# Kernel optimization log

Hardware: AMD Instinct MI355X
Metric: run time of the kernel (lower is better)

## Reference

```python
import jax, jax.numpy as jnp
import numpy as np

N_NODES = 200000
N_EDGES = 4000000

# SE3 layout (pypose convention): [tx, ty, tz, qx, qy, qz, qw]

def _qmul(q, r):
    x1, y1, z1, w1 = q[..., 0], q[..., 1], q[..., 2], q[..., 3]
    x2, y2, z2, w2 = r[..., 0], r[..., 1], r[..., 2], r[..., 3]
    return jnp.stack([
        w1 * x2 + x1 * w2 + y1 * z2 - z1 * y2,
        w1 * y2 - x1 * z2 + y1 * w2 + z1 * x2,
        w1 * z2 + x1 * y2 - y1 * x2 + z1 * w2,
        w1 * w2 - x1 * x2 - y1 * y2 - z1 * z2,
    ], axis=-1)


def _qrot(q, v):
    # rotate vector v by unit quaternion q: v + w*t + qv x t, t = 2 qv x v
    qv, w = q[..., :3], q[..., 3:4]
    t = 2.0 * jnp.cross(qv, v)
    return v + w * t + jnp.cross(qv, t)


def _se3_inv(T):
    t, q = T[..., :3], T[..., 3:]
    qi = q * jnp.asarray([-1.0, -1.0, -1.0, 1.0], dtype=T.dtype)
    ti = -_qrot(qi, t)
    return jnp.concatenate([ti, qi], axis=-1)


def _se3_mul(T1, T2):
    t1, q1 = T1[..., :3], T1[..., 3:]
    t2, q2 = T2[..., :3], T2[..., 3:]
    return jnp.concatenate([t1 + _qrot(q1, t2), _qmul(q1, q2)], axis=-1)


def _se3_log(T):
    # SE3 Log -> se3 [rho(3), phi(3)] (pypose order: translational part first)
    t, q = T[..., :3], T[..., 3:]
    # canonicalize quaternion to w >= 0 (shortest rotation)
    q = jnp.where(q[..., 3:4] < 0, -q, q)
    qv, w = q[..., :3], q[..., 3]
    n = jnp.linalg.norm(qv, axis=-1)           # sin(theta/2)
    theta = 2.0 * jnp.arctan2(n, w)            # rotation angle in [0, pi]
    small = n < 1e-6
    safe_n = jnp.where(small, 1.0, n)
    # phi = theta * axis ; small-angle: 2/w (Taylor of 2*atan2(n,w)/n)
    scale = jnp.where(small, 2.0 / jnp.maximum(w, 1e-12), theta / safe_n)
    phi = scale[..., None] * qv
    # rho = Jl(phi)^{-1} t
    th2 = theta * theta
    tiny = theta < 1e-4
    safe_th = jnp.where(tiny, 1.0, theta)
    coef = jnp.where(
        tiny,
        1.0 / 12.0 + th2 / 720.0,
        1.0 / jnp.where(tiny, 1.0, th2)
        - (1.0 + jnp.cos(safe_th)) / (2.0 * safe_th * jnp.sin(safe_th)),
    )
    pxt = jnp.cross(phi, t)
    rho = t - 0.5 * pxt + coef[..., None] * jnp.cross(phi, pxt)
    return jnp.concatenate([rho, phi], axis=-1)


def _random_se3(key, n):
    kt, kq = jax.random.split(key)
    t = jax.random.normal(kt, (n, 3), dtype=jnp.float32)
    q = jax.random.normal(kq, (n, 4), dtype=jnp.float32)
    q = q / jnp.linalg.norm(q, axis=-1, keepdims=True)
    return jnp.concatenate([t, q], axis=-1)


def setup_inputs() -> dict:
    key = jax.random.key(0)
    k1, k2, k3 = jax.random.split(key, 3)
    nodes = _random_se3(k1, N_NODES)            # [N, 7]
    poses = _random_se3(k2, N_EDGES)            # [E, 7]
    edges = jax.random.randint(k3, (N_EDGES, 2), 0, N_NODES, dtype=jnp.int64)
    return {"nodes": nodes, "poses": poses, "edges": edges}


def reference(nodes, poses, edges):
    node1 = nodes[edges[..., 0]]                # [E, 7] gather
    node2 = nodes[edges[..., 1]]                # [E, 7] gather
    error = _se3_mul(_se3_mul(poses, _se3_inv(node1)), node2)
    return _se3_log(error)                      # [E, 6]
```

## Files before the change

kernel.cpp:

```cpp
#include <hip/hip_runtime.h>

constexpr int BLK = 256;
constexpr int EPT = 2;
constexpr int EPB = BLK * EPT;

struct F3 { float x, y, z; };
struct F4 { float x, y, z, w; };

__device__ __forceinline__ F3 cross3(const F3 a, const F3 b) {
    return { a.y * b.z - a.z * b.y,
             a.z * b.x - a.x * b.z,
             a.x * b.y - a.y * b.x };
}

__device__ __forceinline__ F3 qrot(const F4 q, const F3 v) {
    F3 qv{ q.x, q.y, q.z };
    F3 t = cross3(qv, v);
    t.x *= 2.f; t.y *= 2.f; t.z *= 2.f;
    F3 c = cross3(qv, t);
    return { v.x + q.w * t.x + c.x,
             v.y + q.w * t.y + c.y,
             v.z + q.w * t.z + c.z };
}

__device__ __forceinline__ F4 qmul(const F4 a, const F4 b) {
    return { a.w * b.x + a.x * b.w + a.y * b.z - a.z * b.y,
             a.w * b.y - a.x * b.z + a.y * b.w + a.z * b.x,
             a.w * b.z + a.x * b.y - a.y * b.x + a.z * b.w,
             a.w * b.w - a.x * b.x - a.y * b.y - a.z * b.z };
}

__device__ __forceinline__ void edge_compute(const F3 tp, const F4 qp,
                                             const float4 nA0, const float4 nA1,
                                             const float4 nB0, const float4 nB1,
                                             float* __restrict__ o)
{
    F3 t1{ nA0.x, nA0.y, nA0.z };
    F4 q1{ nA0.w, nA1.x, nA1.y, nA1.z };
    F3 t2{ nB0.x, nB0.y, nB0.z };
    F4 q2{ nB0.w, nB1.x, nB1.y, nB1.z };

    F4 qi{ -q1.x, -q1.y, -q1.z, q1.w };
    F3 ti = qrot(qi, t1);
    ti.x = -ti.x; ti.y = -ti.y; ti.z = -ti.z;

    F3 ra = qrot(qp, ti);
    F3 tA{ tp.x + ra.x, tp.y + ra.y, tp.z + ra.z };
    F4 qA = qmul(qp, qi);

    F3 rb = qrot(qA, t2);
    F3 tE{ tA.x + rb.x, tA.y + rb.y, tA.z + rb.z };
    F4 qE = qmul(qA, q2);

    if (qE.w < 0.f) { qE.x = -qE.x; qE.y = -qE.y; qE.z = -qE.z; qE.w = -qE.w; }
    const float n2q = qE.x * qE.x + qE.y * qE.y + qE.z * qE.z;
    const float nq = sqrtf(n2q);
    const float theta = 2.f * atan2f(nq, qE.w);
    const bool small = nq < 1e-6f;
    const float scale = small ? (2.f / fmaxf(qE.w, 1e-12f)) : (theta / nq);
    const F3 phi{ scale * qE.x, scale * qE.y, scale * qE.z };

    const float th2 = theta * theta;
    float coef;
    if (theta < 1e-4f) {
        coef = 1.f / 12.f + th2 / 720.f;
    } else {
        coef = 1.f / th2 - (1.f + cosf(theta)) / (2.f * theta * sinf(theta));
    }

    const F3 pxt  = cross3(phi, tE);
    const F3 ppxt = cross3(phi, pxt);
    o[0] = tE.x - 0.5f * pxt.x + coef * ppxt.x;
    o[1] = tE.y - 0.5f * pxt.y + coef * ppxt.y;
    o[2] = tE.z - 0.5f * pxt.z + coef * ppxt.z;
    o[3] = phi.x; o[4] = phi.y; o[5] = phi.z;
}

__global__ __launch_bounds__(BLK) void pad_nodes_kernel(
    const float* __restrict__ nodes, float* __restrict__ ws, int n_nodes)
{
    int i = blockIdx.x * BLK + threadIdx.x;
    if (i < n_nodes) {
        const float* s = nodes + (size_t)i * 7;
        float4 a{ s[0], s[1], s[2], s[3] };
        float4 b{ s[4], s[5], s[6], 0.f };
        float4* d = (float4*)(ws + (size_t)i * 8);
        d[0] = a; d[1] = b;
    }
}

template<int NS>
__device__ __forceinline__ void load_node(const float* __restrict__ nodes, int idx,
                                          float4& a, float4& b)
{
    if (NS == 8) {
        const float4* g = (const float4*)(nodes + (size_t)idx * 8);
        a = g[0]; b = g[1];
    } else {
        const float* g = nodes + (size_t)idx * 7;
        a = { g[0], g[1], g[2], g[3] };
        b = { g[4], g[5], g[6], 0.f };
    }
}

template<int NS>
__global__ __launch_bounds__(BLK) void pose_graph_err_kernel(
    const float* __restrict__ nodes,
    const float* __restrict__ poses,
    const int*   __restrict__ edges,
    float*       __restrict__ out,
    int n_edges)
{
    __shared__ float s_pose[EPB * 7];

    const int tid = threadIdx.x;
    const long long bstart = (long long)blockIdx.x * EPB;
    const long long remain = (long long)n_edges - bstart;

    if (remain >= EPB) {
        const float4* pv = (const float4*)(poses + bstart * 7);
        float4* sp = (float4*)s_pose;
        #pragma unroll
        for (int i = tid; i < EPB * 7 / 4; i += BLK) sp[i] = pv[i];

        const long long e0 = bstart + (long long)tid * EPT;
        const int4 ij = *(const int4*)(edges + e0 * 2);

        float4 nA0, nA1, nB0, nB1, nC0, nC1, nD0, nD1;
        load_node<NS>(nodes, ij.x, nA0, nA1);
        load_node<NS>(nodes, ij.y, nB0, nB1);
        load_node<NS>(nodes, ij.z, nC0, nC1);
        load_node<NS>(nodes, ij.w, nD0, nD1);

        __syncthreads();

        const float* p0 = s_pose + tid * 14;
        F3 tp0{ p0[0], p0[1], p0[2] };
        F4 qp0{ p0[3], p0[4], p0[5], p0[6] };
        F3 tp1{ p0[7], p0[8], p0[9] };
        F4 qp1{ p0[10], p0[11], p0[12], p0[13] };

        union { float4 v[3]; float f[12]; } O;
        edge_compute(tp0, qp0, nA0, nA1, nB0, nB1, &O.f[0]);
        edge_compute(tp1, qp1, nC0, nC1, nD0, nD1, &O.f[6]);

        float4* ov = (float4*)(out + e0 * 6);
        ov[0] = O.v[0]; ov[1] = O.v[1]; ov[2] = O.v[2];
    } else {
        for (int k = 0; k < EPT; ++k) {
            const long long e = bstart + tid + (long long)k * BLK;
            if (e < n_edges) {
                const float* sp = poses + e * 7;
                F3 tp{ sp[0], sp[1], sp[2] };
                F4 qp{ sp[3], sp[4], sp[5], sp[6] };
                float4 a0, a1, b0, b1;
                load_node<NS>(nodes, edges[e*2],   a0, a1);
                load_node<NS>(nodes, edges[e*2+1], b0, b1);
                float o[6];
                edge_compute(tp, qp, a0, a1, b0, b1, o);
                #pragma unroll
                for (int j = 0; j < 6; ++j) out[e*6+j] = o[j];
            }
        }
    }
}

extern "C" void kernel_launch(void* const* d_in, const int* in_sizes, int n_in,
                              void* d_out, int out_size, void* d_ws, size_t ws_size,
                              hipStream_t stream) {
    const float* nodes = (const float*)d_in[0];
    const float* poses = (const float*)d_in[1];
    const int*   edges = (const int*)d_in[2];
    float* out = (float*)d_out;

    const int n_nodes = in_sizes[0] / 7;
    const int n_edges = in_sizes[2] / 2;
    const int nblocks = (n_edges + EPB - 1) / EPB;

    const size_t pad_bytes = (size_t)n_nodes * 8 * sizeof(float);
    if (ws_size >= pad_bytes) {
        float* nodes8 = (float*)d_ws;
        pad_nodes_kernel<<<(n_nodes + BLK - 1) / BLK, BLK, 0, stream>>>(nodes, nodes8, n_nodes);
        pose_graph_err_kernel<8><<<nblocks, BLK, 0, stream>>>(nodes8, poses, edges, out, n_edges);
    } else {
        pose_graph_err_kernel<7><<<nblocks, BLK, 0, stream>>>(nodes, poses, edges, out, n_edges);
    }
}
```

Measured before the change: 124.5 us.

## Use one edge per thread, stage outputs in LDS, drop sin/cos in log

Each thread now handles one edge instead of two. Outputs are staged in shared memory and written back with coalesced float4 stores. The rotation coefficient uses the identity (1+cos θ)/sin θ = w/n, taken from the quaternion, so the cosf/sinf calls are no longer needed. This trades the extra per-thread edge parallelism for more blocks and an additional barrier plus an LDS round trip, and it removes costly transcendental calls from the compute path.

```diff
diff --git a/kernel.cpp b/kernel.cpp
--- a/kernel.cpp
+++ b/kernel.cpp
@@ -1,8 +1,6 @@
 #include <hip/hip_runtime.h>
 
 constexpr int BLK = 256;
-constexpr int EPT = 2;
-constexpr int EPB = BLK * EPT;
 
 struct F3 { float x, y, z; };
 struct F4 { float x, y, z, w; };
@@ -56,17 +54,14 @@
     const float n2q = qE.x * qE.x + qE.y * qE.y + qE.z * qE.z;
     const float nq = sqrtf(n2q);
     const float theta = 2.f * atan2f(nq, qE.w);
-    const bool small = nq < 1e-6f;
-    const float scale = small ? (2.f / fmaxf(qE.w, 1e-12f)) : (theta / nq);
+
+    const float scale = (nq < 1e-6f) ? (2.f / fmaxf(qE.w, 1e-12f)) : (theta / nq);
     const F3 phi{ scale * qE.x, scale * qE.y, scale * qE.z };
 
     const float th2 = theta * theta;
-    float coef;
-    if (theta < 1e-4f) {
-        coef = 1.f / 12.f + th2 / 720.f;
-    } else {
-        coef = 1.f / th2 - (1.f + cosf(theta)) / (2.f * theta * sinf(theta));
-    }
+    const float coef = (theta < 1e-4f)
+        ? (1.f / 12.f + th2 / 720.f)
+        : (1.f / th2 - qE.w / (2.f * theta * nq));
 
     const F3 pxt  = cross3(phi, tE);
     const F3 ppxt = cross3(phi, pxt);
@@ -111,57 +106,53 @@
     float*       __restrict__ out,
     int n_edges)
 {
-    __shared__ float s_pose[EPB * 7];
+    __shared__ float s_pose[BLK * 7];
+    __shared__ float s_out [BLK * 6];
 
     const int tid = threadIdx.x;
-    const long long bstart = (long long)blockIdx.x * EPB;
-    const long long remain = (long long)n_edges - bstart;
+    const int bstart = blockIdx.x * BLK;
+    const int cnt = min(BLK, n_edges - bstart);
 
-    if (remain >= EPB) {
-        const float4* pv = (const float4*)(poses + bstart * 7);
+    float4 a0, a1, b0, b1;
+    if (tid < cnt) {
+        const int2 ij = ((const int2*)edges)[bstart + tid];
+        load_node<NS>(nodes, ij.x, a0, a1);
+        load_node<NS>(nodes, ij.y, b0, b1);
+    }
+
+    if (cnt == BLK) {
+        const float4* pv = (const float4*)(poses + (size_t)bstart * 7);
         float4* sp = (float4*)s_pose;
         #pragma unroll
-        for (int i = tid; i < EPB * 7 / 4; i += BLK) sp[i] = pv[i];
+        for (int i = tid; i < BLK * 7 / 4; i += BLK) sp[i] = pv[i];
+    } else {
+        for (int i = tid; i < cnt * 7; i += BLK)
+            s_pose[i] = poses[(size_t)bstart * 7 + i];
+    }
+    __syncthreads();
 
-        const long long e0 = bstart + (long long)tid * EPT;
-        const int4 ij = *(const int4*)(edges + e0 * 2);
+    if (tid < cnt) {
+        const float* sp = s_pose + tid * 7;
+        F3 tp{ sp[0], sp[1], sp[2] };
+        F4 qp{ sp[3], sp[4], sp[5], sp[6] };
 
-        float4 nA0, nA1, nB0, nB1, nC0, nC1, nD0, nD1;
-        load_node<NS>(nodes, ij.x, nA0, nA1);
-        load_node<NS>(nodes, ij.y, nB0, nB1);
-        load_node<NS>(nodes, ij.z, nC0, nC1);
-        load_node<NS>(nodes, ij.w, nD0, nD1);
+        float o[6];
+        edge_compute(tp, qp, a0, a1, b0, b1, o);
 
-        __syncthreads();
+        float* so = s_out + tid * 6;
+        #pragma unroll
+        for (int j = 0; j < 6; ++j) so[j] = o[j];
+    }
+    __syncthreads();
 
-        const float* p0 = s_pose + tid * 14;
-        F3 tp0{ p0[0], p0[1], p0[2] };
-        F4 qp0{ p0[3], p0[4], p0[5], p0[6] };
-        F3 tp1{ p0[7], p0[8], p0[9] };
-        F4 qp1{ p0[10], p0[11], p0[12], p0[13] };
-
-        union { float4 v[3]; float f[12]; } O;
-        edge_compute(tp0, qp0, nA0, nA1, nB0, nB1, &O.f[0]);
-        edge_compute(tp1, qp1, nC0, nC1, nD0, nD1, &O.f[6]);
-
-        float4* ov = (float4*)(out + e0 * 6);
-        ov[0] = O.v[0]; ov[1] = O.v[1]; ov[2] = O.v[2];
+    if (cnt == BLK) {
+        float4* ov = (float4*)(out + (size_t)bstart * 6);
+        const float4* sv = (const float4*)s_out;
+        #pragma unroll
+        for (int i = tid; i < BLK * 6 / 4; i += BLK) ov[i] = sv[i];
     } else {
-        for (int k = 0; k < EPT; ++k) {
-            const long long e = bstart + tid + (long long)k * BLK;
-            if (e < n_edges) {
-                const float* sp = poses + e * 7;
-                F3 tp{ sp[0], sp[1], sp[2] };
-                F4 qp{ sp[3], sp[4], sp[5], sp[6] };
-                float4 a0, a1, b0, b1;
-                load_node<NS>(nodes, edges[e*2],   a0, a1);
-                load_node<NS>(nodes, edges[e*2+1], b0, b1);
-                float o[6];
-                edge_compute(tp, qp, a0, a1, b0, b1, o);
-                #pragma unroll
-                for (int j = 0; j < 6; ++j) out[e*6+j] = o[j];
-            }
-        }
+        for (int i = tid; i < cnt * 6; i += BLK)
+            out[(size_t)bstart * 6 + i] = s_out[i];
     }
 }
 
@@ -175,7 +166,7 @@
 
     const int n_nodes = in_sizes[0] / 7;
     const int n_edges = in_sizes[2] / 2;
-    const int nblocks = (n_edges + EPB - 1) / EPB;
+    const int nblocks = (n_edges + BLK - 1) / BLK;
 
     const size_t pad_bytes = (size_t)n_nodes * 8 * sizeof(float);
     if (ws_size >= pad_bytes) {
```

New measurement: 115.5 us. -7.2%, faster.
